# Kernel optimization log

Measured on AMD Instinct MI355X. Metric: run time of the kernel, lower is better.

Reference implementation:

```python
import jax, jax.numpy as jnp
import numpy as np

N_NODES = 100000
N_EDGES = 300000
N_GRAPHS = 2048
IN_DIM = 38
HID = 256
LAYERS = 5
OUT_DIM = 1
BN_EPS = 1e-5


def setup_inputs() -> dict:
    key = jax.random.key(0)
    ks = jax.random.split(key, 20)
    x = jax.random.normal(ks[0], (N_NODES, IN_DIM), dtype=jnp.float32)
    edge_index = jax.random.randint(ks[1], (2, N_EDGES), 0, N_NODES, dtype=jnp.int32)
    batch = jnp.sort(jax.random.randint(ks[2], (N_NODES,), 0, N_GRAPHS, dtype=jnp.int32))
    s_in = 1.0 / np.sqrt(IN_DIM)
    s_h = 1.0 / np.sqrt(HID)
    return {
        "x": x,
        "edge_index": edge_index,
        "batch": batch,
        "Wp": jax.random.uniform(ks[3], (IN_DIM, HID), jnp.float32, -s_in, s_in),
        "bp": jnp.zeros((HID,), jnp.float32),
        "eps": jnp.zeros((LAYERS,), jnp.float32),  # train_eps=True, init 0
        "W1s": jax.random.uniform(ks[4], (LAYERS, HID, HID), jnp.float32, -s_h, s_h),
        "b1s": jnp.zeros((LAYERS, HID), jnp.float32),
        "W2s": jax.random.uniform(ks[5], (LAYERS, HID, HID), jnp.float32, -s_h, s_h),
        "b2s": jnp.zeros((LAYERS, HID), jnp.float32),
        "gammas": jnp.ones((LAYERS, HID), jnp.float32),
        "betas": jnp.zeros((LAYERS, HID), jnp.float32),
        "Wr1": jax.random.uniform(ks[6], (HID, HID), jnp.float32, -s_h, s_h),
        "br1": jnp.zeros((HID,), jnp.float32),
        "Wr2": jax.random.uniform(ks[7], (HID, OUT_DIM), jnp.float32, -s_h, s_h),
        "br2": jnp.zeros((OUT_DIM,), jnp.float32),
    }


def _forward(x, edge_index, batch, Wp, bp, eps, W1s, b1s, W2s, b2s,
             gammas, betas, Wr1, br1, Wr2, br2):
    src, dst = edge_index[0], edge_index[1]
    h = x @ Wp + bp  # [N, HID]
    for l in range(LAYERS):
        # GINConv: (1+eps)*h_i + sum_{j->i} h_j  (scatter-add over edges)
        agg = jnp.zeros_like(h).at[dst].add(h[src])
        z = (1.0 + eps[l]) * h + agg
        # 2-layer MLP
        z = jax.nn.relu(z @ W1s[l] + b1s[l]) @ W2s[l] + b2s[l]
        # BatchNorm1d (training-mode batch statistics, biased variance)
        mu = jnp.mean(z, axis=0)
        var = jnp.var(z, axis=0)
        z = (z - mu) * jax.lax.rsqrt(var + BN_EPS) * gammas[l] + betas[l]
        h = jax.nn.relu(z)  # dropout disabled (eval)
    # global mean pool over graphs
    sums = jax.ops.segment_sum(h, batch, num_segments=N_GRAPHS)
    counts = jax.ops.segment_sum(jnp.ones((h.shape[0],), h.dtype), batch,
                                 num_segments=N_GRAPHS)
    pooled = sums / jnp.maximum(counts, 1.0)[:, None]
    # readout MLP (dropout disabled)
    out = jax.nn.relu(pooled @ Wr1 + br1) @ Wr2 + br2
    return out  # [N_GRAPHS, OUT_DIM]


def reference(x, edge_index, batch, Wp, bp, eps, W1s, b1s, W2s, b2s,
              gammas, betas, Wr1, br1, Wr2, br2):
    return _forward(x, edge_index, batch, Wp, bp, eps, W1s, b1s, W2s, b2s,
                    gammas, betas, Wr1, br1, Wr2, br2)
```

## Files before the change

kernel.cpp:

```cpp
#include <hip/hip_runtime.h>

#define N_NODES 100000
#define N_EDGES 300000
#define N_GRAPHS 2048
#define IN_DIM 38
#define HID 256
#define LAYERS 5
#define BN_EPS 1e-5f

#define SCAN_CHUNK 512
#define N_CHUNKS ((N_NODES + SCAN_CHUNK - 1) / SCAN_CHUNK)

#define ROW_PAD 128

typedef unsigned short u16;
typedef __attribute__((ext_vector_type(8))) short short8;
typedef __attribute__((ext_vector_type(4))) unsigned short ushortx4;
typedef __attribute__((ext_vector_type(4))) float floatx4;

__device__ __forceinline__ unsigned short bf16_rne(float f) {
    unsigned int u = __float_as_uint(f);
    unsigned int r = (u + 0x7fffu + ((u >> 16) & 1u)) >> 16;
    return (unsigned short)r;
}
__device__ __forceinline__ float uf(unsigned short b) {
    return __uint_as_float((unsigned int)b << 16);
}
__device__ __forceinline__ void split_bf16(float v, unsigned short& hi,
                                           unsigned short& lo) {
    hi = bf16_rne(v);
    float hf = __uint_as_float((unsigned int)hi << 16);
    lo = (unsigned short)(__float_as_uint(v - hf) >> 16);
}
__device__ __forceinline__ void load16_to_lds(const void* g, void* l) {
    __builtin_amdgcn_global_load_lds(
        (const __attribute__((address_space(1))) unsigned int*)g,
        (__attribute__((address_space(3))) unsigned int*)l, 16, 0, 0);
}

#define PROJ_CH 64
__global__ __launch_bounds__(256) void proj_kernel(
    const float* __restrict__ x, const float* __restrict__ Wp,
    const float* __restrict__ bp, u16* __restrict__ h) {
    __shared__ float xs[PROJ_CH * IN_DIM];
    int t = threadIdx.x;
    float w[IN_DIM];
#pragma unroll
    for (int k = 0; k < IN_DIM; k++) w[k] = Wp[k * HID + t];
    float b = bp[t];
    int n0 = blockIdx.x * PROJ_CH;
    int count = min(PROJ_CH, N_NODES - n0);
    int total = count * IN_DIM;
    const float* xbase = x + (size_t)n0 * IN_DIM;
    for (int i = t; i < total; i += 256) xs[i] = xbase[i];
    __syncthreads();
    for (int n = 0; n < count; n++) {
        float acc = b;
        const float* xr = &xs[n * IN_DIM];
#pragma unroll
        for (int k = 0; k < IN_DIM; k++) acc = fmaf(xr[k], w[k], acc);
        unsigned short hb, lb;
        split_bf16(acc, hb, lb);
        h[(size_t)(n0 + n) * 512 + t] = hb;
        h[(size_t)(n0 + n) * 512 + 256 + t] = lb;
    }
}

__global__ __launch_bounds__(256) void hist_kernel(const int* __restrict__ ei,
                                                   int* __restrict__ deg) {
    int e = blockIdx.x * 256 + threadIdx.x;
    if (e < N_EDGES) atomicAdd(&deg[ei[N_EDGES + e]], 1);
}

__global__ __launch_bounds__(256) void scan1_kernel(const int* __restrict__ deg,
                                                    int* __restrict__ offs,
                                                    int* __restrict__ blocksums) {
    __shared__ int s[SCAN_CHUNK];
    int base = blockIdx.x * SCAN_CHUNK;
    int t = threadIdx.x;
    int i0 = t, i1 = t + 256;
    int g0 = base + i0, g1 = base + i1;
    int o0 = (g0 < N_NODES) ? deg[g0] : 0;
    int o1 = (g1 < N_NODES) ? deg[g1] : 0;
    s[i0] = o0;
    s[i1] = o1;
    __syncthreads();
    for (int off = 1; off < SCAN_CHUNK; off <<= 1) {
        int v0 = (i0 >= off) ? s[i0 - off] : 0;
        int v1 = (i1 >= off) ? s[i1 - off] : 0;
        __syncthreads();
        s[i0] += v0;
        s[i1] += v1;
        __syncthreads();
    }
    if (g0 < N_NODES) offs[g0] = s[i0] - o0;
    if (g1 < N_NODES) offs[g1] = s[i1] - o1;
    if (t == 0) blocksums[blockIdx.x] = s[SCAN_CHUNK - 1];
}

__global__ __launch_bounds__(256) void scan2_kernel(int* __restrict__ blocksums) {
    __shared__ int s[256];
    int t = threadIdx.x;
    int o = (t < N_CHUNKS) ? blocksums[t] : 0;
    s[t] = o;
    __syncthreads();
    for (int off = 1; off < 256; off <<= 1) {
        int v = (t >= off) ? s[t - off] : 0;
        __syncthreads();
        s[t] += v;
        __syncthreads();
    }
    if (t < N_CHUNKS) blocksums[t] = s[t] - o;
}

__global__ __launch_bounds__(256) void scan3_kernel(int* __restrict__ offs,
                                                    const int* __restrict__ blocksums,
                                                    int* __restrict__ cursor) {
    int g = blockIdx.x * 256 + threadIdx.x;
    if (g < N_NODES) {
        int v = offs[g] + blocksums[g / SCAN_CHUNK];
        offs[g] = v;
        cursor[g] = v;
    }
    if (g == 0) offs[N_NODES] = N_EDGES;
}

__global__ __launch_bounds__(256) void fill_kernel(const int* __restrict__ ei,
                                                   int* __restrict__ cursor,
                                                   int* __restrict__ csr_src) {
    int e = blockIdx.x * 256 + threadIdx.x;
    if (e < N_EDGES) {
        int src = ei[e];
        int dst = ei[N_EDGES + e];
        int pos = atomicAdd(&cursor[dst], 1);
        csr_src[pos] = src;
    }
}

__global__ __launch_bounds__(256) void gather_kernel(
    const int* __restrict__ offs, const int* __restrict__ csr_src,
    const u16* __restrict__ zin, u16* __restrict__ zout,
    const float* __restrict__ eps, int layer,
    const float* __restrict__ scale, const float* __restrict__ shift,
    int useBN) {
    int wave = threadIdx.x >> 6;
    int lane = threadIdx.x & 63;
    int node = blockIdx.x * 4 + wave;
    if (node >= N_NODES) return;
    float s = 1.0f + eps[layer];
    int c0 = lane * 4;
    float4 sc = make_float4(1.f, 1.f, 1.f, 1.f);
    float4 sh = make_float4(0.f, 0.f, 0.f, 0.f);
    if (useBN) {
        sc = *(const float4*)&scale[c0];
        sh = *(const float4*)&shift[c0];
    }
    int beg = offs[node], end = offs[node + 1];
    float acc[4];
    {
        ushortx4 hi = *(const ushortx4*)&zin[(size_t)node * 512 + c0];
        ushortx4 lo = *(const ushortx4*)&zin[(size_t)node * 512 + 256 + c0];
        acc[0] = uf(hi[0]) + uf(lo[0]);
        acc[1] = uf(hi[1]) + uf(lo[1]);
        acc[2] = uf(hi[2]) + uf(lo[2]);
        acc[3] = uf(hi[3]) + uf(lo[3]);
    }
    if (useBN) {
        acc[0] = fmaxf(acc[0] * sc.x + sh.x, 0.f);
        acc[1] = fmaxf(acc[1] * sc.y + sh.y, 0.f);
        acc[2] = fmaxf(acc[2] * sc.z + sh.z, 0.f);
        acc[3] = fmaxf(acc[3] * sc.w + sh.w, 0.f);
    }
    acc[0] *= s; acc[1] *= s; acc[2] *= s; acc[3] *= s;
    for (int e = beg; e < end; e++) {
        int src = csr_src[e];
        ushortx4 hi = *(const ushortx4*)&zin[(size_t)src * 512 + c0];
        ushortx4 lo = *(const ushortx4*)&zin[(size_t)src * 512 + 256 + c0];
        float v0 = uf(hi[0]) + uf(lo[0]);
        float v1 = uf(hi[1]) + uf(lo[1]);
        float v2 = uf(hi[2]) + uf(lo[2]);
        float v3 = uf(hi[3]) + uf(lo[3]);
        if (useBN) {
            v0 = fmaxf(v0 * sc.x + sh.x, 0.f);
            v1 = fmaxf(v1 * sc.y + sh.y, 0.f);
            v2 = fmaxf(v2 * sc.z + sh.z, 0.f);
            v3 = fmaxf(v3 * sc.w + sh.w, 0.f);
        }
        acc[0] += v0; acc[1] += v1; acc[2] += v2; acc[3] += v3;
    }
    ushortx4 ho, lo2;
#pragma unroll
    for (int e = 0; e < 4; e++) {
        unsigned short hb, lb;
        split_bf16(acc[e], hb, lb);
        ho[e] = hb;
        lo2[e] = lb;
    }
    *(ushortx4*)&zout[(size_t)node * 512 + c0] = ho;
    *(ushortx4*)&zout[(size_t)node * 512 + 256 + c0] = lo2;
}

__global__ __launch_bounds__(256) void packW_kernel(const float* __restrict__ W1s,
                                                    const float* __restrict__ W2s,
                                                    short8* __restrict__ Wpk8) {
    int id = blockIdx.x * 256 + threadIdx.x;
    int lane = id & 63;
    int fid = (id >> 6) & 127;
    int w = id >> 13;
    int kt = fid >> 4, nt = fid & 15;
    const float* Wsrc = (w < 5) ? W1s + (size_t)w * HID * HID
                                : W2s + (size_t)(w - 5) * HID * HID;
    int k0 = kt * 32 + ((lane >> 4) << 3);
    int n = nt * 16 + (lane & 15);
    short8 hi, lo;
#pragma unroll
    for (int e = 0; e < 8; e++) {
        float v = Wsrc[(size_t)(k0 + e) * HID + n];
        unsigned short hb, lb;
        split_bf16(v, hb, lb);
        hi[e] = (short)hb;
        lo[e] = (short)lb;
    }
    size_t base = (size_t)w * 16384;
    Wpk8[base + (size_t)((0 * 8 + kt) * 16 + nt) * 64 + lane] = hi;
    Wpk8[base + (size_t)((1 * 8 + kt) * 16 + nt) * 64 + lane] = lo;
}

__global__ __launch_bounds__(256, 2) void fused_mlp_kernel(
    const u16* __restrict__ A, const short8* __restrict__ W1m,
    const float* __restrict__ b1, const short8* __restrict__ W2m,
    const float* __restrict__ b2, u16* __restrict__ C, int M,
    float* __restrict__ sums, float* __restrict__ sumsq) {
    __shared__ char lds[65536];
    short8* As8 = (short8*)lds;
    u16* Hf = (u16*)lds;
    float* cf = (float*)lds;
    int t = threadIdx.x;
    int lane = t & 63;
    int w = t >> 6;
    int m0 = blockIdx.x * 64;
    int col15 = lane & 15;
    int rgrp = lane >> 4;

    floatx4 acc[4][4];
#pragma unroll
    for (int i = 0; i < 4; i++)
#pragma unroll
        for (int j = 0; j < 4; j++) acc[i][j] = (floatx4)0.0f;

    for (int ki = 0; ki < 4; ki++) {
#pragma unroll
        for (int q = 0; q < 4; q++) {
            int f = q * 4 + w;
            int p = f >> 3, ktl = (f >> 2) & 1, mt = f & 3;
            const u16* src = &A[(size_t)(m0 + mt * 16 + col15) * 512 + p * 256 +
                                ki * 64 + ktl * 32 + (rgrp << 3)];
            load16_to_lds(src, &As8[f * 64]);
        }
        short8 bb[2][2][4];
#pragma unroll
        for (int p = 0; p < 2; p++)
#pragma unroll
            for (int ktl = 0; ktl < 2; ktl++)
#pragma unroll
                for (int j = 0; j < 4; j++)
                    bb[p][ktl][j] =
                        W1m[((size_t)(p * 8 + ki * 2 + ktl) * 16 + (w * 4 + j)) *
                                64 +
                            lane];
        __syncthreads();
#pragma unroll
        for (int ktl = 0; ktl < 2; ktl++) {
            short8 ah[4], al[4];
#pragma unroll
            for (int mt = 0; mt < 4; mt++) {
                ah[mt] = As8[(0 * 8 + ktl * 4 + mt) * 64 + lane];
                al[mt] = As8[(1 * 8 + ktl * 4 + mt) * 64 + lane];
            }
#pragma unroll
            for (int i = 0; i < 4; i++)
#pragma unroll
                for (int j = 0; j < 4; j++) {
                    acc[i][j] = __builtin_amdgcn_mfma_f32_16x16x32_bf16(
                        ah[i], bb[0][ktl][j], acc[i][j], 0, 0, 0);
                    acc[i][j] = __builtin_amdgcn_mfma_f32_16x16x32_bf16(
                        ah[i], bb[1][ktl][j], acc[i][j], 0, 0, 0);
                    acc[i][j] = __builtin_amdgcn_mfma_f32_16x16x32_bf16(
                        al[i], bb[0][ktl][j], acc[i][j], 0, 0, 0);
                }
        }
        __syncthreads();
    }

#pragma unroll
    for (int j = 0; j < 4; j++) {
        int col = w * 64 + j * 16 + col15;
        float bv = b1[col];
        int kt2 = col >> 5;
        int colg = (col & 31) >> 3;
        int e = col & 7;
#pragma unroll
        for (int i = 0; i < 4; i++) {
            int lane_a = rgrp * 4 + colg * 16;
#pragma unroll
            for (int r = 0; r < 4; r++) {
                float v = fmaxf(acc[i][j][r] + bv, 0.0f);
                unsigned short hb, lb;
                split_bf16(v, hb, lb);
                Hf[(((0 * 8 + kt2) * 4 + i) * 64 + lane_a + r) * 8 + e] = hb;
                Hf[(((1 * 8 + kt2) * 4 + i) * 64 + lane_a + r) * 8 + e] = lb;
            }
        }
    }
    __syncthreads();

    floatx4 acc2[4][4];
#pragma unroll
    for (int i = 0; i < 4; i++)
#pragma unroll
        for (int j = 0; j < 4; j++) acc2[i][j] = (floatx4)0.0f;

#pragma unroll
    for (int kj = 0; kj < 8; kj++) {
        short8 bb2[2][4];
#pragma unroll
        for (int p = 0; p < 2; p++)
#pragma unroll
            for (int j = 0; j < 4; j++)
                bb2[p][j] =
                    W2m[((size_t)(p * 8 + kj) * 16 + (w * 4 + j)) * 64 + lane];
        short8 ah2[4], al2[4];
#pragma unroll
        for (int mt = 0; mt < 4; mt++) {
            ah2[mt] = *(short8*)&Hf[(((0 * 8 + kj) * 4 + mt) * 64 + lane) * 8];
            al2[mt] = *(short8*)&Hf[(((1 * 8 + kj) * 4 + mt) * 64 + lane) * 8];
        }
#pragma unroll
        for (int i = 0; i < 4; i++)
#pragma unroll
            for (int j = 0; j < 4; j++) {
                acc2[i][j] = __builtin_amdgcn_mfma_f32_16x16x32_bf16(
                    ah2[i], bb2[0][j], acc2[i][j], 0, 0, 0);
                acc2[i][j] = __builtin_amdgcn_mfma_f32_16x16x32_bf16(
                    ah2[i], bb2[1][j], acc2[i][j], 0, 0, 0);
                acc2[i][j] = __builtin_amdgcn_mfma_f32_16x16x32_bf16(
                    al2[i], bb2[0][j], acc2[i][j], 0, 0, 0);
            }
    }
    __syncthreads();

#pragma unroll
    for (int j = 0; j < 4; j++) {
        int col = w * 64 + j * 16 + col15;
        float bv = b2[col];
        float csum = 0.f, csq = 0.f;
#pragma unroll
        for (int i = 0; i < 4; i++) {
            int rowb = i * 16 + rgrp * 4;
#pragma unroll
            for (int r = 0; r < 4; r++) {
                float v = acc2[i][j][r] + bv;
                cf[(rowb + r) * 256 + col] = v;
                if (m0 + rowb + r < M) {
                    csum += v;
                    csq += v * v;
                }
            }
        }
        csum += __shfl_xor(csum, 16);
        csum += __shfl_xor(csum, 32);
        csq += __shfl_xor(csq, 16);
        csq += __shfl_xor(csq, 32);
        if (rgrp == 0) {
            atomicAdd(&sums[col], csum);
            atomicAdd(&sumsq[col], csq);
        }
    }
    __syncthreads();
#pragma unroll
    for (int k = 0; k < 16; k++) {
        int fi = (k * 256 + t) * 4;
        int row = fi >> 8, colc = fi & 255;
        int m = m0 + row;
        if (m >= M) continue;
        float4 v4 = *(float4*)&cf[fi];
        ushortx4 h4, l4;
        unsigned short hb, lb;
        split_bf16(v4.x, hb, lb); h4[0] = hb; l4[0] = lb;
        split_bf16(v4.y, hb, lb); h4[1] = hb; l4[1] = lb;
        split_bf16(v4.z, hb, lb); h4[2] = hb; l4[2] = lb;
        split_bf16(v4.w, hb, lb); h4[3] = hb; l4[3] = lb;
        *(ushortx4*)&C[(size_t)m * 512 + colc] = h4;
        *(ushortx4*)&C[(size_t)m * 512 + 256 + colc] = l4;
    }
}

__global__ void bnparams_kernel(const float* __restrict__ sums,
                                const float* __restrict__ sumsq,
                                const float* __restrict__ gammas,
                                const float* __restrict__ betas, int layer,
                                float* __restrict__ scale,
                                float* __restrict__ shift) {
    int c = threadIdx.x;
    float mu = sums[c] / (float)N_NODES;
    float var = sumsq[c] / (float)N_NODES - mu * mu;
    float rs = rsqrtf(var + BN_EPS);
    float g = gammas[layer * HID + c];
    scale[c] = rs * g;
    shift[c] = betas[layer * HID + c] - mu * rs * g;
}

__global__ __launch_bounds__(256) void bounds_kernel(const int* __restrict__ batch,
                                                     int* __restrict__ start) {
    int g = blockIdx.x * 256 + threadIdx.x;
    if (g > N_GRAPHS) return;
    int lo = 0, hi = N_NODES;
    while (lo < hi) {
        int mid = (lo + hi) >> 1;
        if (batch[mid] < g) lo = mid + 1;
        else hi = mid;
    }
    start[g] = lo;
}

__global__ __launch_bounds__(256) void segpool_kernel(
    const u16* __restrict__ z, const int* __restrict__ start,
    const float* __restrict__ scale, const float* __restrict__ shift,
    float* __restrict__ pooled) {
    int g = blockIdx.x;
    int c = threadIdx.x;
    float sc = scale[c], sh = shift[c];
    int beg = start[g], end = start[g + 1];
    float s = 0.f;
    for (int n = beg; n < end; n++) {
        float v = uf(z[(size_t)n * 512 + c]) + uf(z[(size_t)n * 512 + 256 + c]);
        s += fmaxf(v * sc + sh, 0.f);
    }
    float inv = 1.0f / fmaxf((float)(end - beg), 1.0f);
    pooled[(size_t)g * HID + c] = s * inv;
}

__global__ __launch_bounds__(256) void readout_kernel(
    const float* __restrict__ pooled, const float* __restrict__ Wr1,
    const float* __restrict__ br1, const float* __restrict__ Wr2,
    const float* __restrict__ br2, float* __restrict__ out) {
    __shared__ float p[HID];
    __shared__ float red[4];
    int g = blockIdx.x;
    int c = threadIdx.x;
    p[c] = pooled[(size_t)g * HID + c];
    __syncthreads();
    float acc = br1[c];
    for (int k = 0; k < HID; k++) acc += p[k] * Wr1[k * HID + c];
    acc = fmaxf(acc, 0.f);
    float v = acc * Wr2[c];
#pragma unroll
    for (int off = 32; off > 0; off >>= 1) v += __shfl_down(v, off, 64);
    if ((c & 63) == 0) red[c >> 6] = v;
    __syncthreads();
    if (c == 0) out[g] = red[0] + red[1] + red[2] + red[3] + br2[0];
}

extern "C" void kernel_launch(void* const* d_in, const int* in_sizes, int n_in,
                              void* d_out, int out_size, void* d_ws, size_t ws_size,
                              hipStream_t stream) {
    const float* x      = (const float*)d_in[0];
    const int*   ei     = (const int*)d_in[1];
    const int*   batch  = (const int*)d_in[2];
    const float* Wp     = (const float*)d_in[3];
    const float* bp     = (const float*)d_in[4];
    const float* eps    = (const float*)d_in[5];
    const float* W1s    = (const float*)d_in[6];
    const float* b1s    = (const float*)d_in[7];
    const float* W2s    = (const float*)d_in[8];
    const float* b2s    = (const float*)d_in[9];
    const float* gammas = (const float*)d_in[10];
    const float* betas  = (const float*)d_in[11];
    const float* Wr1    = (const float*)d_in[12];
    const float* br1    = (const float*)d_in[13];
    const float* Wr2    = (const float*)d_in[14];
    const float* br2    = (const float*)d_in[15];
    float* out = (float*)d_out;

    const size_t ROWS = (size_t)N_NODES + ROW_PAD;
    u16* bufA     = (u16*)d_ws;
    u16* bufB     = bufA + ROWS * 512;
    short8* Wpk8  = (short8*)(bufB + ROWS * 512);
    float* sums   = (float*)(Wpk8 + 10 * 16384);
    float* sumsq  = sums + HID;
    float* scale  = sumsq + HID;
    float* shift  = scale + HID;
    float* pooled = shift + HID;
    int* start     = (int*)(pooled + (size_t)N_GRAPHS * HID);
    int* deg       = start + N_GRAPHS + 1;
    int* offs      = deg + N_NODES;
    int* cursor    = offs + N_NODES + 1;
    int* csr_src   = cursor + N_NODES;
    int* blocksums = csr_src + N_EDGES;

    hipMemsetAsync(deg, 0, N_NODES * sizeof(int), stream);
    hist_kernel<<<(N_EDGES + 255) / 256, 256, 0, stream>>>(ei, deg);
    scan1_kernel<<<N_CHUNKS, 256, 0, stream>>>(deg, offs, blocksums);
    scan2_kernel<<<1, 256, 0, stream>>>(blocksums);
    scan3_kernel<<<(N_NODES + 255) / 256, 256, 0, stream>>>(offs, blocksums,
                                                            cursor);
    fill_kernel<<<(N_EDGES + 255) / 256, 256, 0, stream>>>(ei, cursor, csr_src);
    packW_kernel<<<320, 256, 0, stream>>>(W1s, W2s, Wpk8);
    bounds_kernel<<<(N_GRAPHS + 1 + 255) / 256, 256, 0, stream>>>(batch, start);

    proj_kernel<<<(N_NODES + PROJ_CH - 1) / PROJ_CH, 256, 0, stream>>>(x, Wp, bp,
                                                                       bufA);

    const int MLP_BLOCKS = (N_NODES + 63) / 64;
    for (int l = 0; l < LAYERS; l++) {
        hipMemsetAsync(sums, 0, 2 * HID * sizeof(float), stream);
        gather_kernel<<<(N_NODES + 3) / 4, 256, 0, stream>>>(
            offs, csr_src, bufA, bufB, eps, l, scale, shift, l > 0 ? 1 : 0);
        fused_mlp_kernel<<<MLP_BLOCKS, 256, 0, stream>>>(
            bufB, Wpk8 + (size_t)l * 16384, b1s + l * HID,
            Wpk8 + (size_t)(5 + l) * 16384, b2s + l * HID, bufA, N_NODES,
            sums, sumsq);
        bnparams_kernel<<<1, HID, 0, stream>>>(sums, sumsq, gammas, betas, l,
                                               scale, shift);
    }

    segpool_kernel<<<N_GRAPHS, 256, 0, stream>>>(bufA, start, scale, shift,
                                                 pooled);
    readout_kernel<<<N_GRAPHS, 256, 0, stream>>>(pooled, Wr1, br1, Wr2, br2, out);
}
```

Measured before the change: 1.103 ms.

## Fuse neighbor gather into MLP kernel, staging aggregated rows in LDS

The separate gather kernel is removed. Each MLP block now aggregates its 64 nodes' neighbor features straight into LDS in the MFMA fragment layout before the first GEMM, and the two node buffers are ping-ponged. This drops the write and re-read of the intermediate aggregated tensor and one launch per layer. The cost is that each wave gathers 16 nodes serially inside a block limited by launch bounds and LDS usage, so latency hiding on the random gathers may be worse than in the dedicated gather kernel.

```diff
diff --git a/kernel.cpp b/kernel.cpp
--- a/kernel.cpp
+++ b/kernel.cpp
@@ -31,11 +31,6 @@
     hi = bf16_rne(v);
     float hf = __uint_as_float((unsigned int)hi << 16);
     lo = (unsigned short)(__float_as_uint(v - hf) >> 16);
-}
-__device__ __forceinline__ void load16_to_lds(const void* g, void* l) {
-    __builtin_amdgcn_global_load_lds(
-        (const __attribute__((address_space(1))) unsigned int*)g,
-        (__attribute__((address_space(3))) unsigned int*)l, 16, 0, 0);
 }
 
 #define PROJ_CH 64
@@ -135,69 +130,6 @@
         int pos = atomicAdd(&cursor[dst], 1);
         csr_src[pos] = src;
     }
-}
-
-__global__ __launch_bounds__(256) void gather_kernel(
-    const int* __restrict__ offs, const int* __restrict__ csr_src,
-    const u16* __restrict__ zin, u16* __restrict__ zout,
-    const float* __restrict__ eps, int layer,
-    const float* __restrict__ scale, const float* __restrict__ shift,
-    int useBN) {
-    int wave = threadIdx.x >> 6;
-    int lane = threadIdx.x & 63;
-    int node = blockIdx.x * 4 + wave;
-    if (node >= N_NODES) return;
-    float s = 1.0f + eps[layer];
-    int c0 = lane * 4;
-    float4 sc = make_float4(1.f, 1.f, 1.f, 1.f);
-    float4 sh = make_float4(0.f, 0.f, 0.f, 0.f);
-    if (useBN) {
-        sc = *(const float4*)&scale[c0];
-        sh = *(const float4*)&shift[c0];
-    }
-    int beg = offs[node], end = offs[node + 1];
-    float acc[4];
-    {
-        ushortx4 hi = *(const ushortx4*)&zin[(size_t)node * 512 + c0];
-        ushortx4 lo = *(const ushortx4*)&zin[(size_t)node * 512 + 256 + c0];
-        acc[0] = uf(hi[0]) + uf(lo[0]);
-        acc[1] = uf(hi[1]) + uf(lo[1]);
-        acc[2] = uf(hi[2]) + uf(lo[2]);
-        acc[3] = uf(hi[3]) + uf(lo[3]);
-    }
-    if (useBN) {
-        acc[0] = fmaxf(acc[0] * sc.x + sh.x, 0.f);
-        acc[1] = fmaxf(acc[1] * sc.y + sh.y, 0.f);
-        acc[2] = fmaxf(acc[2] * sc.z + sh.z, 0.f);
-        acc[3] = fmaxf(acc[3] * sc.w + sh.w, 0.f);
-    }
-    acc[0] *= s; acc[1] *= s; acc[2] *= s; acc[3] *= s;
-    for (int e = beg; e < end; e++) {
-        int src = csr_src[e];
-        ushortx4 hi = *(const ushortx4*)&zin[(size_t)src * 512 + c0];
-        ushortx4 lo = *(const ushortx4*)&zin[(size_t)src * 512 + 256 + c0];
-        float v0 = uf(hi[0]) + uf(lo[0]);
-        float v1 = uf(hi[1]) + uf(lo[1]);
-        float v2 = uf(hi[2]) + uf(lo[2]);
-        float v3 = uf(hi[3]) + uf(lo[3]);
-        if (useBN) {
-            v0 = fmaxf(v0 * sc.x + sh.x, 0.f);
-            v1 = fmaxf(v1 * sc.y + sh.y, 0.f);
-            v2 = fmaxf(v2 * sc.z + sh.z, 0.f);
-            v3 = fmaxf(v3 * sc.w + sh.w, 0.f);
-        }
-        acc[0] += v0; acc[1] += v1; acc[2] += v2; acc[3] += v3;
-    }
-    ushortx4 ho, lo2;
-#pragma unroll
-    for (int e = 0; e < 4; e++) {
-        unsigned short hb, lb;
-        split_bf16(acc[e], hb, lb);
-        ho[e] = hb;
-        lo2[e] = lb;
-    }
-    *(ushortx4*)&zout[(size_t)node * 512 + c0] = ho;
-    *(ushortx4*)&zout[(size_t)node * 512 + 256 + c0] = lo2;
 }
 
 __global__ __launch_bounds__(256) void packW_kernel(const float* __restrict__ W1s,
@@ -226,13 +158,17 @@
     Wpk8[base + (size_t)((1 * 8 + kt) * 16 + nt) * 64 + lane] = lo;
 }
 
-__global__ __launch_bounds__(256, 2) void fused_mlp_kernel(
-    const u16* __restrict__ A, const short8* __restrict__ W1m,
-    const float* __restrict__ b1, const short8* __restrict__ W2m,
-    const float* __restrict__ b2, u16* __restrict__ C, int M,
+__global__ __launch_bounds__(256, 2) void fused_layer_kernel(
+    const u16* __restrict__ zin, const int* __restrict__ offs,
+    const int* __restrict__ csr_src, const float* __restrict__ eps, int layer,
+    const float* __restrict__ scale, const float* __restrict__ shift, int useBN,
+    const short8* __restrict__ W1m, const float* __restrict__ b1,
+    const short8* __restrict__ W2m, const float* __restrict__ b2,
+    u16* __restrict__ zout, int M,
     float* __restrict__ sums, float* __restrict__ sumsq) {
     __shared__ char lds[65536];
-    short8* As8 = (short8*)lds;
+    short8* Zf8 = (short8*)lds;
+    u16* Zfu = (u16*)lds;
     u16* Hf = (u16*)lds;
     float* cf = (float*)lds;
     int t = threadIdx.x;
@@ -242,55 +178,110 @@
     int col15 = lane & 15;
     int rgrp = lane >> 4;
 
+    {
+        float s = 1.0f + eps[layer];
+        int c0 = lane * 4;
+        float4 sc = make_float4(1.f, 1.f, 1.f, 1.f);
+        float4 sh = make_float4(0.f, 0.f, 0.f, 0.f);
+        if (useBN) {
+            sc = *(const float4*)&scale[c0];
+            sh = *(const float4*)&shift[c0];
+        }
+        int ki = c0 >> 6;
+        int ktl = (c0 >> 5) & 1;
+        int colg = (c0 >> 3) & 3;
+        int e = c0 & 7;
+        for (int n = 0; n < 16; n++) {
+            int node = m0 + w * 16 + n;
+            float a0 = 0.f, a1 = 0.f, a2 = 0.f, a3 = 0.f;
+            if (node < M) {
+                ushortx4 hi = *(const ushortx4*)&zin[(size_t)node * 512 + c0];
+                ushortx4 lo =
+                    *(const ushortx4*)&zin[(size_t)node * 512 + 256 + c0];
+                a0 = uf(hi[0]) + uf(lo[0]);
+                a1 = uf(hi[1]) + uf(lo[1]);
+                a2 = uf(hi[2]) + uf(lo[2]);
+                a3 = uf(hi[3]) + uf(lo[3]);
+                if (useBN) {
+                    a0 = fmaxf(a0 * sc.x + sh.x, 0.f);
+                    a1 = fmaxf(a1 * sc.y + sh.y, 0.f);
+                    a2 = fmaxf(a2 * sc.z + sh.z, 0.f);
+                    a3 = fmaxf(a3 * sc.w + sh.w, 0.f);
+                }
+                a0 *= s; a1 *= s; a2 *= s; a3 *= s;
+                int beg = offs[node], end = offs[node + 1];
+                for (int ed = beg; ed < end; ed++) {
+                    int src = csr_src[ed];
+                    ushortx4 vh = *(const ushortx4*)&zin[(size_t)src * 512 + c0];
+                    ushortx4 vl =
+                        *(const ushortx4*)&zin[(size_t)src * 512 + 256 + c0];
+                    float v0 = uf(vh[0]) + uf(vl[0]);
+                    float v1 = uf(vh[1]) + uf(vl[1]);
+                    float v2 = uf(vh[2]) + uf(vl[2]);
+                    float v3 = uf(vh[3]) + uf(vl[3]);
+                    if (useBN) {
+                        v0 = fmaxf(v0 * sc.x + sh.x, 0.f);
+                        v1 = fmaxf(v1 * sc.y + sh.y, 0.f);
+                        v2 = fmaxf(v2 * sc.z + sh.z, 0.f);
+                        v3 = fmaxf(v3 * sc.w + sh.w, 0.f);
+                    }
+                    a0 += v0; a1 += v1; a2 += v2; a3 += v3;
+                }
+            }
+            ushortx4 ho, lo4;
+            unsigned short hb, lb;
+            split_bf16(a0, hb, lb); ho[0] = hb; lo4[0] = lb;
+            split_bf16(a1, hb, lb); ho[1] = hb; lo4[1] = lb;
+            split_bf16(a2, hb, lb); ho[2] = hb; lo4[2] = lb;
+            split_bf16(a3, hb, lb); ho[3] = hb; lo4[3] = lb;
+            int la = n + 16 * colg;
+            int gh = ki * 8 + ktl * 4 + w;
+            *(ushortx4*)&Zfu[((gh)*64 + la) * 8 + e] = ho;
+            *(ushortx4*)&Zfu[((32 + gh) * 64 + la) * 8 + e] = lo4;
+        }
+    }
+    __syncthreads();
+
     floatx4 acc[4][4];
 #pragma unroll
     for (int i = 0; i < 4; i++)
 #pragma unroll
         for (int j = 0; j < 4; j++) acc[i][j] = (floatx4)0.0f;
 
+#pragma unroll
     for (int ki = 0; ki < 4; ki++) {
 #pragma unroll
-        for (int q = 0; q < 4; q++) {
-            int f = q * 4 + w;
-            int p = f >> 3, ktl = (f >> 2) & 1, mt = f & 3;
-            const u16* src = &A[(size_t)(m0 + mt * 16 + col15) * 512 + p * 256 +
-                                ki * 64 + ktl * 32 + (rgrp << 3)];
-            load16_to_lds(src, &As8[f * 64]);
-        }
-        short8 bb[2][2][4];
-#pragma unroll
-        for (int p = 0; p < 2; p++)
-#pragma unroll
-            for (int ktl = 0; ktl < 2; ktl++)
-#pragma unroll
-                for (int j = 0; j < 4; j++)
-                    bb[p][ktl][j] =
-                        W1m[((size_t)(p * 8 + ki * 2 + ktl) * 16 + (w * 4 + j)) *
-                                64 +
-                            lane];
-        __syncthreads();
-#pragma unroll
         for (int ktl = 0; ktl < 2; ktl++) {
+            short8 bb0[4], bb1[4];
+#pragma unroll
+            for (int j = 0; j < 4; j++) {
+                bb0[j] = W1m[((size_t)(0 * 8 + ki * 2 + ktl) * 16 + (w * 4 + j)) *
+                                 64 +
+                             lane];
+                bb1[j] = W1m[((size_t)(1 * 8 + ki * 2 + ktl) * 16 + (w * 4 + j)) *
+                                 64 +
+                             lane];
+            }
             short8 ah[4], al[4];
 #pragma unroll
             for (int mt = 0; mt < 4; mt++) {
-                ah[mt] = As8[(0 * 8 + ktl * 4 + mt) * 64 + lane];
-                al[mt] = As8[(1 * 8 + ktl * 4 + mt) * 64 + lane];
+                ah[mt] = Zf8[(ki * 8 + ktl * 4 + mt) * 64 + lane];
+                al[mt] = Zf8[(32 + ki * 8 + ktl * 4 + mt) * 64 + lane];
             }
 #pragma unroll
             for (int i = 0; i < 4; i++)
 #pragma unroll
                 for (int j = 0; j < 4; j++) {
                     acc[i][j] = __builtin_amdgcn_mfma_f32_16x16x32_bf16(
-                        ah[i], bb[0][ktl][j], acc[i][j], 0, 0, 0);
+                        ah[i], bb0[j], acc[i][j], 0, 0, 0);
                     acc[i][j] = __builtin_amdgcn_mfma_f32_16x16x32_bf16(
-                        ah[i], bb[1][ktl][j], acc[i][j], 0, 0, 0);
+                        ah[i], bb1[j], acc[i][j], 0, 0, 0);
                     acc[i][j] = __builtin_amdgcn_mfma_f32_16x16x32_bf16(
-                        al[i], bb[0][ktl][j], acc[i][j], 0, 0, 0);
+                        al[i], bb0[j], acc[i][j], 0, 0, 0);
                 }
         }
-        __syncthreads();
-    }
+    }
+    __syncthreads();
 
 #pragma unroll
     for (int j = 0; j < 4; j++) {
@@ -390,8 +381,8 @@
         split_bf16(v4.y, hb, lb); h4[1] = hb; l4[1] = lb;
         split_bf16(v4.z, hb, lb); h4[2] = hb; l4[2] = lb;
         split_bf16(v4.w, hb, lb); h4[3] = hb; l4[3] = lb;
-        *(ushortx4*)&C[(size_t)m * 512 + colc] = h4;
-        *(ushortx4*)&C[(size_t)m * 512 + 256 + colc] = l4;
+        *(ushortx4*)&zout[(size_t)m * 512 + colc] = h4;
+        *(ushortx4*)&zout[(size_t)m * 512 + 256 + colc] = l4;
     }
 }
 
@@ -511,20 +502,22 @@
     proj_kernel<<<(N_NODES + PROJ_CH - 1) / PROJ_CH, 256, 0, stream>>>(x, Wp, bp,
                                                                        bufA);
 
+    u16* cur = bufA;
+    u16* nxt = bufB;
     const int MLP_BLOCKS = (N_NODES + 63) / 64;
     for (int l = 0; l < LAYERS; l++) {
         hipMemsetAsync(sums, 0, 2 * HID * sizeof(float), stream);
-        gather_kernel<<<(N_NODES + 3) / 4, 256, 0, stream>>>(
-            offs, csr_src, bufA, bufB, eps, l, scale, shift, l > 0 ? 1 : 0);
-        fused_mlp_kernel<<<MLP_BLOCKS, 256, 0, stream>>>(
-            bufB, Wpk8 + (size_t)l * 16384, b1s + l * HID,
-            Wpk8 + (size_t)(5 + l) * 16384, b2s + l * HID, bufA, N_NODES,
+        fused_layer_kernel<<<MLP_BLOCKS, 256, 0, stream>>>(
+            cur, offs, csr_src, eps, l, scale, shift, l > 0 ? 1 : 0,
+            Wpk8 + (size_t)l * 16384, b1s + l * HID,
+            Wpk8 + (size_t)(5 + l) * 16384, b2s + l * HID, nxt, N_NODES,
             sums, sumsq);
         bnparams_kernel<<<1, HID, 0, stream>>>(sums, sumsq, gammas, betas, l,
                                                scale, shift);
-    }
-
-    segpool_kernel<<<N_GRAPHS, 256, 0, stream>>>(bufA, start, scale, shift,
+        u16* tmp = cur; cur = nxt; nxt = tmp;
+    }
+
+    segpool_kernel<<<N_GRAPHS, 256, 0, stream>>>(cur, start, scale, shift,
                                                  pooled);
     readout_kernel<<<N_GRAPHS, 256, 0, stream>>>(pooled, Wr1, br1, Wr2, br2, out);
 }
```

Result: slower. 1.403 ms (+27.1%).

## Fold BN params into consumers, per-layer stat buffers, single-shot A tile load

Applied to the files above, without the earlier changes.

Removes the per-layer bnparams kernel and the per-layer memset. Gather and segpool now recompute the BN scale and shift directly from the per-layer sums, and all layer statistics buffers are zeroed once at the start. The fused MLP kernel now loads the whole 64-row A tile (hi and lo halves) into LDS in one pass with a single barrier, instead of four K-step loads each with its own syncs. The intent is fewer launches and barriers, at the cost of redundant rsqrt work in every gather wave and less overlap between global loads and MFMA work.

```diff
diff --git a/kernel.cpp b/kernel.cpp
--- a/kernel.cpp
+++ b/kernel.cpp
@@ -36,6 +36,18 @@
     __builtin_amdgcn_global_load_lds(
         (const __attribute__((address_space(1))) unsigned int*)g,
         (__attribute__((address_space(3))) unsigned int*)l, 16, 0, 0);
+}
+__device__ __forceinline__ void bn_params(const float* sums, const float* sumsq,
+                                          const float* gammas,
+                                          const float* betas, int c, float& sc,
+                                          float& sh) {
+    const float invN = 1.0f / (float)N_NODES;
+    float mu = sums[c] * invN;
+    float var = sumsq[c] * invN - mu * mu;
+    float rs = rsqrtf(var + BN_EPS);
+    float g = gammas[c];
+    sc = rs * g;
+    sh = betas[c] - mu * rs * g;
 }
 
 #define PROJ_CH 64
@@ -141,7 +153,8 @@
     const int* __restrict__ offs, const int* __restrict__ csr_src,
     const u16* __restrict__ zin, u16* __restrict__ zout,
     const float* __restrict__ eps, int layer,
-    const float* __restrict__ scale, const float* __restrict__ shift,
+    const float* __restrict__ sums, const float* __restrict__ sumsq,
+    const float* __restrict__ gammas, const float* __restrict__ betas,
     int useBN) {
     int wave = threadIdx.x >> 6;
     int lane = threadIdx.x & 63;
@@ -152,8 +165,10 @@
     float4 sc = make_float4(1.f, 1.f, 1.f, 1.f);
     float4 sh = make_float4(0.f, 0.f, 0.f, 0.f);
     if (useBN) {
-        sc = *(const float4*)&scale[c0];
-        sh = *(const float4*)&shift[c0];
+        bn_params(sums, sumsq, gammas, betas, c0 + 0, sc.x, sh.x);
+        bn_params(sums, sumsq, gammas, betas, c0 + 1, sc.y, sh.y);
+        bn_params(sums, sumsq, gammas, betas, c0 + 2, sc.z, sh.z);
+        bn_params(sums, sumsq, gammas, betas, c0 + 3, sc.w, sh.w);
     }
     int beg = offs[node], end = offs[node + 1];
     float acc[4];
@@ -232,7 +247,7 @@
     const float* __restrict__ b2, u16* __restrict__ C, int M,
     float* __restrict__ sums, float* __restrict__ sumsq) {
     __shared__ char lds[65536];
-    short8* As8 = (short8*)lds;
+    short8* Zf8 = (short8*)lds;
     u16* Hf = (u16*)lds;
     float* cf = (float*)lds;
     int t = threadIdx.x;
@@ -242,55 +257,53 @@
     int col15 = lane & 15;
     int rgrp = lane >> 4;
 
+#pragma unroll
+    for (int q = 0; q < 16; q++) {
+        int f = q * 4 + w;
+        int p = f >> 5;
+        int ki = (f >> 3) & 3;
+        int ktl = (f >> 2) & 1;
+        int mt = f & 3;
+        const u16* src = &A[(size_t)(m0 + mt * 16 + col15) * 512 + p * 256 +
+                            ki * 64 + ktl * 32 + (rgrp << 3)];
+        load16_to_lds(src, &Zf8[f * 64]);
+    }
+    __syncthreads();
+
     floatx4 acc[4][4];
 #pragma unroll
     for (int i = 0; i < 4; i++)
 #pragma unroll
         for (int j = 0; j < 4; j++) acc[i][j] = (floatx4)0.0f;
 
-    for (int ki = 0; ki < 4; ki++) {
-#pragma unroll
-        for (int q = 0; q < 4; q++) {
-            int f = q * 4 + w;
-            int p = f >> 3, ktl = (f >> 2) & 1, mt = f & 3;
-            const u16* src = &A[(size_t)(m0 + mt * 16 + col15) * 512 + p * 256 +
-                                ki * 64 + ktl * 32 + (rgrp << 3)];
-            load16_to_lds(src, &As8[f * 64]);
-        }
-        short8 bb[2][2][4];
-#pragma unroll
-        for (int p = 0; p < 2; p++)
-#pragma unroll
-            for (int ktl = 0; ktl < 2; ktl++)
-#pragma unroll
-                for (int j = 0; j < 4; j++)
-                    bb[p][ktl][j] =
-                        W1m[((size_t)(p * 8 + ki * 2 + ktl) * 16 + (w * 4 + j)) *
-                                64 +
-                            lane];
-        __syncthreads();
-#pragma unroll
-        for (int ktl = 0; ktl < 2; ktl++) {
-            short8 ah[4], al[4];
-#pragma unroll
-            for (int mt = 0; mt < 4; mt++) {
-                ah[mt] = As8[(0 * 8 + ktl * 4 + mt) * 64 + lane];
-                al[mt] = As8[(1 * 8 + ktl * 4 + mt) * 64 + lane];
+#pragma unroll
+    for (int kk = 0; kk < 8; kk++) {
+        int ki = kk >> 1, ktl = kk & 1;
+        short8 bb0[4], bb1[4];
+#pragma unroll
+        for (int j = 0; j < 4; j++) {
+            bb0[j] = W1m[((size_t)(0 * 8 + kk) * 16 + (w * 4 + j)) * 64 + lane];
+            bb1[j] = W1m[((size_t)(1 * 8 + kk) * 16 + (w * 4 + j)) * 64 + lane];
+        }
+        short8 ah[4], al[4];
+#pragma unroll
+        for (int mt = 0; mt < 4; mt++) {
+            ah[mt] = Zf8[((0 << 5) + ki * 8 + ktl * 4 + mt) * 64 + lane];
+            al[mt] = Zf8[((1 << 5) + ki * 8 + ktl * 4 + mt) * 64 + lane];
+        }
+#pragma unroll
+        for (int i = 0; i < 4; i++)
+#pragma unroll
+            for (int j = 0; j < 4; j++) {
+                acc[i][j] = __builtin_amdgcn_mfma_f32_16x16x32_bf16(
+                    ah[i], bb0[j], acc[i][j], 0, 0, 0);
+                acc[i][j] = __builtin_amdgcn_mfma_f32_16x16x32_bf16(
+                    ah[i], bb1[j], acc[i][j], 0, 0, 0);
+                acc[i][j] = __builtin_amdgcn_mfma_f32_16x16x32_bf16(
+                    al[i], bb0[j], acc[i][j], 0, 0, 0);
             }
-#pragma unroll
-            for (int i = 0; i < 4; i++)
-#pragma unroll
-                for (int j = 0; j < 4; j++) {
-                    acc[i][j] = __builtin_amdgcn_mfma_f32_16x16x32_bf16(
-                        ah[i], bb[0][ktl][j], acc[i][j], 0, 0, 0);
-                    acc[i][j] = __builtin_amdgcn_mfma_f32_16x16x32_bf16(
-                        ah[i], bb[1][ktl][j], acc[i][j], 0, 0, 0);
-                    acc[i][j] = __builtin_amdgcn_mfma_f32_16x16x32_bf16(
-                        al[i], bb[0][ktl][j], acc[i][j], 0, 0, 0);
-                }
-        }
-        __syncthreads();
-    }
+    }
+    __syncthreads();
 
 #pragma unroll
     for (int j = 0; j < 4; j++) {
@@ -395,21 +408,6 @@
     }
 }
 
-__global__ void bnparams_kernel(const float* __restrict__ sums,
-                                const float* __restrict__ sumsq,
-                                const float* __restrict__ gammas,
-                                const float* __restrict__ betas, int layer,
-                                float* __restrict__ scale,
-                                float* __restrict__ shift) {
-    int c = threadIdx.x;
-    float mu = sums[c] / (float)N_NODES;
-    float var = sumsq[c] / (float)N_NODES - mu * mu;
-    float rs = rsqrtf(var + BN_EPS);
-    float g = gammas[layer * HID + c];
-    scale[c] = rs * g;
-    shift[c] = betas[layer * HID + c] - mu * rs * g;
-}
-
 __global__ __launch_bounds__(256) void bounds_kernel(const int* __restrict__ batch,
                                                      int* __restrict__ start) {
     int g = blockIdx.x * 256 + threadIdx.x;
@@ -425,11 +423,13 @@
 
 __global__ __launch_bounds__(256) void segpool_kernel(
     const u16* __restrict__ z, const int* __restrict__ start,
-    const float* __restrict__ scale, const float* __restrict__ shift,
+    const float* __restrict__ sums, const float* __restrict__ sumsq,
+    const float* __restrict__ gammas, const float* __restrict__ betas,
     float* __restrict__ pooled) {
     int g = blockIdx.x;
     int c = threadIdx.x;
-    float sc = scale[c], sh = shift[c];
+    float sc, sh;
+    bn_params(sums, sumsq, gammas, betas, c, sc, sh);
     int beg = start[g], end = start[g + 1];
     float s = 0.f;
     for (int n = beg; n < end; n++) {
@@ -487,10 +487,7 @@
     u16* bufB     = bufA + ROWS * 512;
     short8* Wpk8  = (short8*)(bufB + ROWS * 512);
     float* sums   = (float*)(Wpk8 + 10 * 16384);
-    float* sumsq  = sums + HID;
-    float* scale  = sumsq + HID;
-    float* shift  = scale + HID;
-    float* pooled = shift + HID;
+    float* pooled = sums + LAYERS * 512;
     int* start     = (int*)(pooled + (size_t)N_GRAPHS * HID);
     int* deg       = start + N_GRAPHS + 1;
     int* offs      = deg + N_NODES;
@@ -499,6 +496,7 @@
     int* blocksums = csr_src + N_EDGES;
 
     hipMemsetAsync(deg, 0, N_NODES * sizeof(int), stream);
+    hipMemsetAsync(sums, 0, LAYERS * 512 * sizeof(float), stream);
     hist_kernel<<<(N_EDGES + 255) / 256, 256, 0, stream>>>(ei, deg);
     scan1_kernel<<<N_CHUNKS, 256, 0, stream>>>(deg, offs, blocksums);
     scan2_kernel<<<1, 256, 0, stream>>>(blocksums);
@@ -513,18 +511,22 @@
 
     const int MLP_BLOCKS = (N_NODES + 63) / 64;
     for (int l = 0; l < LAYERS; l++) {
-        hipMemsetAsync(sums, 0, 2 * HID * sizeof(float), stream);
+        float* lsums = sums + l * 512;
+        float* lsumsq = lsums + 256;
+        const float* psums = sums + (l - 1) * 512;
         gather_kernel<<<(N_NODES + 3) / 4, 256, 0, stream>>>(
-            offs, csr_src, bufA, bufB, eps, l, scale, shift, l > 0 ? 1 : 0);
+            offs, csr_src, bufA, bufB, eps, l,
+            l > 0 ? psums : sums, l > 0 ? psums + 256 : sums,
+            gammas + (l > 0 ? (l - 1) : 0) * HID,
+            betas + (l > 0 ? (l - 1) : 0) * HID, l > 0 ? 1 : 0);
         fused_mlp_kernel<<<MLP_BLOCKS, 256, 0, stream>>>(
             bufB, Wpk8 + (size_t)l * 16384, b1s + l * HID,
             Wpk8 + (size_t)(5 + l) * 16384, b2s + l * HID, bufA, N_NODES,
-            sums, sumsq);
-        bnparams_kernel<<<1, HID, 0, stream>>>(sums, sumsq, gammas, betas, l,
-                                               scale, shift);
-    }
-
-    segpool_kernel<<<N_GRAPHS, 256, 0, stream>>>(bufA, start, scale, shift,
-                                                 pooled);
+            lsums, lsumsq);
+    }
+
+    segpool_kernel<<<N_GRAPHS, 256, 0, stream>>>(
+        bufA, start, sums + 4 * 512, sums + 4 * 512 + 256, gammas + 4 * HID,
+        betas + 4 * HID, pooled);
     readout_kernel<<<N_GRAPHS, 256, 0, stream>>>(pooled, Wr1, br1, Wr2, br2, out);
 }
```

New measurement: 1.109 ms. Within noise of the previous version (+0.6%).
